# Optimization experiments

Hardware: AMD Instinct MI355X
Metric: run time of the kernel (lower is better)

## Reference

```python
import jax, jax.numpy as jnp
import numpy as np
import math

B, CIN, COUT, K, R = 8, 128, 128, 7, 2
GC = 16                     # group_channels (init arg `groups`)
G = COUT // GC              # number of dynamic-weight groups = 8
H = W = 32
EPS = 1e-5


def c4_lift(w):
    # w: [o, i, 4] -> dense 1x1 weight [o*4, i*4] via cyclic C4 shifts
    # torch: weight[:, r] = w[..., roll-by-r]  (e.g. r=1 -> [3,0,1,2])
    Wr = jnp.stack([jnp.roll(w, r, axis=-1) for r in range(4)], axis=1)  # [o,4,i,4]
    o, _, i, _ = Wr.shape
    return Wr.reshape(o * 4, i * 4)


def setup_inputs() -> dict:
    key = jax.random.key(0)
    ks = jax.random.split(key, 4)
    sc = 1.0 / math.sqrt(4 * CIN / 2)
    x = jax.random.normal(ks[0], (B, CIN * 4, H, W), dtype=jnp.float32)
    v_w = jax.random.normal(ks[1], (COUT, CIN, 4), dtype=jnp.float32) * sc
    c1_w = jax.random.normal(ks[2], (CIN // R, CIN, 4), dtype=jnp.float32) * sc
    gn_g = jnp.ones((CIN // R * 4,), jnp.float32)
    gn_b = jnp.zeros((CIN // R * 4,), jnp.float32)
    c2_w = jax.random.normal(ks[3], (K * K * G, CIN // R), dtype=jnp.float32) * (1.0 / math.sqrt(CIN // R))
    c2_b = jnp.zeros((K * K * G,), jnp.float32)
    return {"x": x, "v_w": v_w, "c1_w": c1_w, "gn_g": gn_g, "gn_b": gn_b, "c2_w": c2_w, "c2_b": c2_b}


def _forward(x, v_w, c1_w, gn_g, gn_b, c2_w, c2_b):
    b, _, h, w = x.shape
    # conv1: C4-equivariant 1x1
    t = jnp.einsum('oc,bchw->bohw', c4_lift(c1_w), x)        # [b, (CIN//R)*4, h, w]
    # GroupNorm(num_groups=CIN//R) -> normalize each group of 4 channels over (4,h,w)
    tr = t.reshape(b, CIN // R, 4, h, w)
    mu = tr.mean(axis=(2, 3, 4), keepdims=True)
    var = tr.var(axis=(2, 3, 4), keepdims=True)
    t = ((tr - mu) * jax.lax.rsqrt(var + EPS)).reshape(b, CIN // R * 4, h, w)
    t = jax.nn.relu(t * gn_g[None, :, None, None] + gn_b[None, :, None, None])
    # conv2: Conv3d 1x1 over the (c, 4) view
    tv = t.reshape(b, CIN // R, 4, h, w)
    wmap = jnp.einsum('oc,bcrhw->borhw', c2_w, tv) + c2_b[None, :, None, None, None]
    wmap = wmap.reshape(b, G, K, K, 4, h, w)
    # rotate the KxK kernel by r*90deg for C4 element r (r=0 identity)
    wmap = jnp.stack([jnp.rot90(wmap[:, :, :, :, r], k=r, axes=(2, 3)) for r in range(4)], axis=4)
    wmap = wmap.reshape(b, G, K * K, 4, h, w)                 # [b, g, p, r, h, w]
    # v branch (C4 1x1) + unfold (im2col, pad (K-1)//2, stride 1)
    v = jnp.einsum('oc,bchw->bohw', c4_lift(v_w), x)          # [b, COUT*4, h, w]
    p = (K - 1) // 2
    vp = jnp.pad(v, ((0, 0), (0, 0), (p, p), (p, p)))
    patches = jnp.stack([vp[:, :, i:i + h, j:j + w] for i in range(K) for j in range(K)], axis=2)
    patches = patches.reshape(b, G, GC, 4, K * K, h, w)       # [b, g, c, r, p, h, w]
    out = jnp.einsum('bgprhw,bgcrphw->bgcrhw', wmap, patches)
    return out.reshape(b, COUT * 4, h, w)


def reference(x, v_w, c1_w, gn_g, gn_b, c2_w, c2_b):
    return _forward(x, v_w, c1_w, gn_g, gn_b, c2_w, c2_b)
```

## Files before the change

### kernel.cpp

```cpp
#include <hip/hip_runtime.h>

#define BB   8
#define CIN  128
#define COUT 128
#define KS   7
#define HH   32
#define WWID 32
#define HW   1024
#define NG   8
#define GC   16
#define MROWS 768
#define TROWS 256
#define VROWS 512
#define KDIM 512
#define WMAP_O 392
#define WMAP_OP 448
#define C2K  64

#define AS1 __attribute__((address_space(1)))
#define AS3 __attribute__((address_space(3)))

typedef __attribute__((ext_vector_type(8))) short bf16x8;
typedef __attribute__((ext_vector_type(4))) float f32x4;

__device__ __forceinline__ short f2bf(float f) {
    unsigned u = __builtin_bit_cast(unsigned, f);
    u += 0x7fff + ((u >> 16) & 1);
    return (short)(u >> 16);
}
__device__ __forceinline__ float bf2f(unsigned short u) {
    unsigned v = (unsigned)u << 16;
    return __builtin_bit_cast(float, v);
}

__global__ __launch_bounds__(256) void prep_kernel(
    const float* __restrict__ x, const float* __restrict__ v_w,
    const float* __restrict__ c1_w, const float* __restrict__ c2_w,
    const float* __restrict__ c2_b,
    short* __restrict__ XT, short* __restrict__ Wb,
    short* __restrict__ c2wb, float* __restrict__ c2bp,
    float* __restrict__ gnstat)
{
    __shared__ short t[64][66];
    int bx = blockIdx.x, tid = threadIdx.x;
    if (bx < 1024) {
        int b = bx >> 7, c0 = ((bx >> 4) & 7) * 64, n0 = (bx & 15) * 64;
        const float* xb = x + ((size_t)b * KDIM + c0) * HW + n0;
        #pragma unroll
        for (int l = 0; l < 16; ++l) {
            int flat = l * 256 + tid;
            int row = flat >> 6, col = flat & 63;
            t[col][row] = f2bf(xb[(size_t)row * HW + col]);
        }
        __syncthreads();
        short* xt = XT + ((size_t)b * HW + n0) * KDIM + c0;
        #pragma unroll
        for (int l = 0; l < 8; ++l) {
            int u = l * 256 + tid;
            int nrow = u >> 5, cp = (u & 31) * 2;
            short2 v = make_short2(t[nrow][cp], t[nrow][cp + 1]);
            *(short2*)(xt + (size_t)nrow * KDIM + cp) = v;
        }
    } else if (bx < 2560) {
        int idx = (bx - 1024) * 256 + tid;
        int row = idx >> 9, col = idx & 511;
        int i = col >> 2, s = col & 3;
        float val;
        if (row < 256) {
            int o = row >> 2, r = row & 3;
            val = c1_w[(o * CIN + i) * 4 + ((s - r) & 3)];
        } else {
            int ro = row - 256;
            int o = ro >> 2, r = ro & 3;
            val = v_w[(o * CIN + i) * 4 + ((s - r) & 3)];
        }
        Wb[idx] = f2bf(val);
    } else if (bx < 2672) {
        int idx = (bx - 2560) * 256 + tid;
        int o = idx >> 6, k = idx & 63;
        c2wb[idx] = f2bf(o < WMAP_O ? c2_w[o * C2K + k] : 0.f);
        if (idx < WMAP_OP)
            c2bp[idx] = idx < WMAP_O ? c2_b[idx] : 0.f;
    } else {
        *(float4*)(gnstat + tid * 4) = make_float4(0.f, 0.f, 0.f, 0.f);
    }
}

#define GBM 64
#define GBN 128
#define GBK 64
__global__ __launch_bounds__(256) void gemm_mfma_kernel(
    const short* __restrict__ Wb, const short* __restrict__ XT,
    short* __restrict__ tvb, float* __restrict__ gnstat)
{
    __shared__ short As[2][GBM * GBK];
    __shared__ short Bs[2][GBN * GBK];
    int b  = blockIdx.z;
    int m0 = blockIdx.y * GBM;
    int n0 = blockIdx.x * GBN;
    int tid = threadIdx.x;
    int lane = tid & 63, wv = tid >> 6;
    int wm = wv & 1, wn = wv >> 1;
    int rl = lane & 15, kg = lane >> 4;
    const short* Ab = Wb + (size_t)m0 * KDIM;
    const short* Bb = XT + ((size_t)b * HW + n0) * KDIM;
    f32x4 acc[2][4] = {};

#define GEMM_STAGE(buf, k0)                                                              \
    do {                                                                                 \
        _Pragma("unroll")                                                                \
        for (int l = 0; l < 2; ++l) {                                                    \
            int c = l * 256 + tid;                                                       \
            int row = c >> 3, kc = c & 7;                                                \
            int kcs = kc ^ (row & 7);                                                    \
            __builtin_amdgcn_global_load_lds(                                            \
                (const AS1 void*)(Ab + (size_t)row * KDIM + (k0) + kcs * 8),             \
                (AS3 void*)(As[buf] + (l * 256 + wv * 64) * 8), 16, 0, 0);               \
        }                                                                                \
        _Pragma("unroll")                                                                \
        for (int l = 0; l < 4; ++l) {                                                    \
            int c = l * 256 + tid;                                                       \
            int row = c >> 3, kc = c & 7;                                                \
            int kcs = kc ^ (row & 7);                                                    \
            __builtin_amdgcn_global_load_lds(                                            \
                (const AS1 void*)(Bb + (size_t)row * KDIM + (k0) + kcs * 8),             \
                (AS3 void*)(Bs[buf] + (l * 256 + wv * 64) * 8), 16, 0, 0);               \
        }                                                                                \
    } while (0)

    GEMM_STAGE(0, 0);
    __syncthreads();
    for (int t = 0; t < KDIM / GBK; ++t) {
        int cur = t & 1;
        if (t < KDIM / GBK - 1) GEMM_STAGE(cur ^ 1, (t + 1) * GBK);
        #pragma unroll
        for (int ks = 0; ks < 2; ++ks) {
            bf16x8 af[2], bfr[4];
            #pragma unroll
            for (int mf = 0; mf < 2; ++mf) {
                int row = wm * 32 + mf * 16 + rl;
                af[mf] = *(const bf16x8*)(As[cur] + row * GBK + ((ks * 4 + kg) ^ (row & 7)) * 8);
            }
            #pragma unroll
            for (int nf = 0; nf < 4; ++nf) {
                int row = wn * 64 + nf * 16 + rl;
                bfr[nf] = *(const bf16x8*)(Bs[cur] + row * GBK + ((ks * 4 + kg) ^ (row & 7)) * 8);
            }
            #pragma unroll
            for (int mf = 0; mf < 2; ++mf)
                #pragma unroll
                for (int nf = 0; nf < 4; ++nf)
                    acc[mf][nf] = __builtin_amdgcn_mfma_f32_16x16x32_bf16(af[mf], bfr[nf], acc[mf][nf], 0, 0, 0);
        }
        __syncthreads();
    }
#undef GEMM_STAGE

    short* Cb = tvb + (size_t)b * MROWS * HW;
    #pragma unroll
    for (int mf = 0; mf < 2; ++mf) {
        int rowb = m0 + wm * 32 + mf * 16 + kg * 4;
        #pragma unroll
        for (int nf = 0; nf < 4; ++nf) {
            int col = n0 + wn * 64 + nf * 16 + rl;
            #pragma unroll
            for (int i = 0; i < 4; ++i)
                Cb[(size_t)(rowb + i) * HW + col] = f2bf(acc[mf][nf][i]);
        }
    }

    if (m0 < TROWS) {
        #pragma unroll
        for (int mf = 0; mf < 2; ++mf) {
            float s = 0.f, sq = 0.f;
            #pragma unroll
            for (int nf = 0; nf < 4; ++nf)
                #pragma unroll
                for (int i = 0; i < 4; ++i) {
                    float v = acc[mf][nf][i];
                    s += v; sq += v * v;
                }
            #pragma unroll
            for (int m = 1; m <= 8; m <<= 1) {
                s  += __shfl_xor(s, m);
                sq += __shfl_xor(sq, m);
            }
            if (rl == 0) {
                int grp = (m0 + wm * 32 + mf * 16 + kg * 4) >> 2;
                atomicAdd(&gnstat[(b * 64 + grp) * 2],     s);
                atomicAdd(&gnstat[(b * 64 + grp) * 2 + 1], sq);
            }
        }
    }
}

__global__ __launch_bounds__(256) void tkn2_kernel(
    const short* __restrict__ tvb, const float* __restrict__ gnstat,
    const float* __restrict__ gn_g, const float* __restrict__ gn_b,
    short* __restrict__ tn)
{
    __shared__ short ts[64][72];
    __shared__ float sc[64], sh[64];
    int b4r = blockIdx.x;
    int b = b4r >> 2, r = b4r & 3;
    int hw0 = blockIdx.y * 64;
    int tid = threadIdx.x;
    if (tid < 64) {
        float s   = gnstat[(b * 64 + tid) * 2];
        float sq  = gnstat[(b * 64 + tid) * 2 + 1];
        float mu  = s * (1.f / 4096.f);
        float var = sq * (1.f / 4096.f) - mu * mu;
        float inv = rsqrtf(var + 1e-5f);
        int ch = tid * 4 + r;
        float g = gn_g[ch], bb = gn_b[ch];
        sc[tid] = inv * g;
        sh[tid] = bb - mu * inv * g;
    }
    #pragma unroll
    for (int l = 0; l < 16; ++l) {
        int flat = l * 256 + tid;
        int c = flat >> 6, hw = flat & 63;
        ts[c][hw] = tvb[((size_t)b * MROWS + c * 4 + r) * HW + hw0 + hw];
    }
    __syncthreads();
    #pragma unroll
    for (int l = 0; l < 2; ++l) {
        int u = l * 256 + tid;
        int hw = u >> 3, c0 = (u & 7) * 8;
        bf16x8 v;
        #pragma unroll
        for (int j = 0; j < 8; ++j) {
            float f = bf2f((unsigned short)ts[c0 + j][hw]);
            f = fmaxf(f * sc[c0 + j] + sh[c0 + j], 0.f);
            v[j] = f2bf(f);
        }
        *(bf16x8*)(tn + ((size_t)b4r * HW + hw0 + hw) * C2K + c0) = v;
    }
}

__global__ __launch_bounds__(256) void wmap3_kernel(
    const short* __restrict__ c2wb, const short* __restrict__ tn,
    const float* __restrict__ c2bp, short* __restrict__ wmapB)
{
    __shared__ short As[64 * 64];
    __shared__ short Bs[128 * 64];
    int n0  = blockIdx.x * 128;
    int m0  = blockIdx.y * 64;
    int b4r = blockIdx.z;
    int tid = threadIdx.x;
    int lane = tid & 63, wv = tid >> 6;
    int wm = wv & 1, wn = wv >> 1;
    int rl = lane & 15, kg = lane >> 4;
    const short* Bb = tn + ((size_t)b4r * HW + n0) * C2K;

    #pragma unroll
    for (int l = 0; l < 2; ++l) {
        int c = l * 256 + tid;
        int row = c >> 3, kc = c & 7;
        int kcs = kc ^ (row & 7);
        __builtin_amdgcn_global_load_lds(
            (const AS1 void*)(c2wb + (size_t)(m0 + row) * C2K + kcs * 8),
            (AS3 void*)(As + (l * 256 + wv * 64) * 8), 16, 0, 0);
    }
    #pragma unroll
    for (int l = 0; l < 4; ++l) {
        int c = l * 256 + tid;
        int row = c >> 3, kc = c & 7;
        int kcs = kc ^ (row & 7);
        __builtin_amdgcn_global_load_lds(
            (const AS1 void*)(Bb + (size_t)row * C2K + kcs * 8),
            (AS3 void*)(Bs + (l * 256 + wv * 64) * 8), 16, 0, 0);
    }
    __syncthreads();

    f32x4 acc[2][4] = {};
    #pragma unroll
    for (int ks = 0; ks < 2; ++ks) {
        bf16x8 af[2], bfr[4];
        #pragma unroll
        for (int mf = 0; mf < 2; ++mf) {
            int row = wm * 32 + mf * 16 + rl;
            af[mf] = *(const bf16x8*)(As + row * 64 + ((ks * 4 + kg) ^ (row & 7)) * 8);
        }
        #pragma unroll
        for (int nf = 0; nf < 4; ++nf) {
            int row = wn * 64 + nf * 16 + rl;
            bfr[nf] = *(const bf16x8*)(Bs + row * 64 + ((ks * 4 + kg) ^ (row & 7)) * 8);
        }
        #pragma unroll
        for (int mf = 0; mf < 2; ++mf)
            #pragma unroll
            for (int nf = 0; nf < 4; ++nf)
                acc[mf][nf] = __builtin_amdgcn_mfma_f32_16x16x32_bf16(af[mf], bfr[nf], acc[mf][nf], 0, 0, 0);
    }

    short* wb = wmapB + (size_t)b4r * WMAP_OP * HW;
    #pragma unroll
    for (int mf = 0; mf < 2; ++mf) {
        int rowb = m0 + wm * 32 + mf * 16 + kg * 4;
        float bi[4];
        #pragma unroll
        for (int i = 0; i < 4; ++i) bi[i] = c2bp[rowb + i];
        #pragma unroll
        for (int nf = 0; nf < 4; ++nf) {
            int col = n0 + wn * 64 + nf * 16 + rl;
            #pragma unroll
            for (int i = 0; i < 4; ++i)
                wb[(size_t)(rowb + i) * HW + col] = f2bf(acc[mf][nf][i] + bi[i]);
        }
    }
}

__global__ __launch_bounds__(256, 3) void agg5_kernel(
    const short* __restrict__ tvb, const short* __restrict__ wmapB,
    float* __restrict__ out)
{
    __shared__ float vt[16][15][44];
    int bx = blockIdx.x;
    int b = bx >> 5;
    int g = (bx >> 2) & 7;
    int r = bx & 3;
    int h0  = blockIdx.y * 8;
    int tid = threadIdx.x;
    int w0q = tid & 7, hb = (tid >> 3) & 1, cc4 = (tid >> 4) & 3, cq = tid >> 6;
    int hl = cq * 2 + hb;
    int h = h0 + hl, w0 = w0q * 4;

    int A, Bc, Cc;
    if      (r == 0) { A = 0;  Bc = 7;  Cc = 1;  }
    else if (r == 1) { A = 6;  Bc = -1; Cc = 7;  }
    else if (r == 2) { A = 48; Bc = -7; Cc = -1; }
    else             { A = 42; Bc = 1;  Cc = -7; }

    const short* vpb = tvb + ((size_t)b * MROWS + TROWS) * HW;
    for (int e = tid; e < 16 * 15 * 3; e += 256) {
        int cc  = e / 45;
        int rem = e - cc * 45;
        int row = rem / 3, q = rem - row * 3;
        int col = (q == 0) ? 0 : (36 + (q - 1) * 4);
        *(float4*)(&vt[cc][row][col]) = make_float4(0.f, 0.f, 0.f, 0.f);
    }
    for (int f = tid; f < 16 * 15 * 8; f += 256) {
        int cc  = f / 120;
        int rem = f - cc * 120;
        int row = rem >> 3, q = rem & 7;
        int gh = h0 - 3 + row;
        float4 v4 = make_float4(0.f, 0.f, 0.f, 0.f);
        if (gh >= 0 && gh < HH) {
            int ch = (g * GC + cc) * 4 + r;
            ushort4 u = *(const ushort4*)(vpb + (size_t)ch * HW + gh * WWID + q * 4);
            v4 = make_float4(bf2f(u.x), bf2f(u.y), bf2f(u.z), bf2f(u.w));
        }
        *(float4*)(&vt[cc][row][4 + q * 4]) = v4;
    }
    __syncthreads();

    const short* wmb = wmapB + ((size_t)(b * 4 + r) * WMAP_OP + g * 49) * HW + h * WWID + w0;
    float acc[4][4] = {};
    #pragma unroll
    for (int di = 0; di < 7; ++di) {
        float wrf[7][4];
        #pragma unroll
        for (int dj = 0; dj < 7; ++dj) {
            int porig = A + Bc * di + Cc * dj;
            ushort4 wv = *(const ushort4*)(wmb + (size_t)porig * HW);
            wrf[dj][0] = bf2f(wv.x); wrf[dj][1] = bf2f(wv.y);
            wrf[dj][2] = bf2f(wv.z); wrf[dj][3] = bf2f(wv.w);
        }
        #pragma unroll
        for (int c2 = 0; c2 < 4; ++c2) {
            int hc = cc4 * 4 + c2;
            const float* rp = &vt[hc][hl + di][w0];
            float4 q0 = *(const float4*)(rp);
            float4 q1 = *(const float4*)(rp + 4);
            float4 q2 = *(const float4*)(rp + 8);
            float win[12] = {q0.x, q0.y, q0.z, q0.w,
                             q1.x, q1.y, q1.z, q1.w,
                             q2.x, q2.y, q2.z, q2.w};
            #pragma unroll
            for (int dj = 0; dj < 7; ++dj)
                #pragma unroll
                for (int px = 0; px < 4; ++px)
                    acc[c2][px] += wrf[dj][px] * win[px + dj + 1];
        }
    }
    #pragma unroll
    for (int c2 = 0; c2 < 4; ++c2) {
        int ch = (g * GC + cc4 * 4 + c2) * 4 + r;
        float4 o4 = make_float4(acc[c2][0], acc[c2][1], acc[c2][2], acc[c2][3]);
        *(float4*)(out + ((size_t)b * 512 + ch) * HW + h * WWID + w0) = o4;
    }
}

extern "C" void kernel_launch(void* const* d_in, const int* in_sizes, int n_in,
                              void* d_out, int out_size, void* d_ws, size_t ws_size,
                              hipStream_t stream)
{
    const float* x    = (const float*)d_in[0];
    const float* v_w  = (const float*)d_in[1];
    const float* c1_w = (const float*)d_in[2];
    const float* gn_g = (const float*)d_in[3];
    const float* gn_b = (const float*)d_in[4];
    const float* c2_w = (const float*)d_in[5];
    const float* c2_b = (const float*)d_in[6];
    float* out = (float*)d_out;

    char* p = (char*)d_ws;
    short* Wb     = (short*)p;           p += (size_t)MROWS * KDIM * 2;
    short* tvb    = (short*)p;           p += (size_t)BB * MROWS * HW * 2;
    short* wmapB  = (short*)p;           p += (size_t)32 * WMAP_OP * HW * 2;
    short* XT     = (short*)wmapB;
    short* tn     = (short*)p;           p += (size_t)32 * HW * C2K * 2;
    short* c2wb   = (short*)p;           p += (size_t)WMAP_OP * C2K * 2;
    float* c2bp   = (float*)p;           p += (size_t)WMAP_OP * 4;
    float* gnstat = (float*)p;           p += (size_t)512 * 2 * 4;

    prep_kernel     <<<2673, 256, 0, stream>>>(x, v_w, c1_w, c2_w, c2_b, XT, Wb, c2wb, c2bp, gnstat);
    gemm_mfma_kernel<<<dim3(HW / GBN, MROWS / GBM, BB), 256, 0, stream>>>(Wb, XT, tvb, gnstat);
    tkn2_kernel     <<<dim3(32, 16), 256, 0, stream>>>(tvb, gnstat, gn_g, gn_b, tn);
    wmap3_kernel    <<<dim3(HW / 128, WMAP_OP / 64, 32), 256, 0, stream>>>(c2wb, tn, c2bp, wmapB);
    agg5_kernel     <<<dim3(BB * NG * 4, 4), 256, 0, stream>>>(tvb, wmapB, out);
}
```

Baseline: 64.33 us.

## Stage wmap GEMM output through LDS for coalesced stores; split aggregation channels

The wmap GEMM epilogue now writes the bf16 results into shared memory and then stores them to global memory as contiguous 16-byte rows. It also skips the padded rows past 392. Previously each lane wrote scattered 2-byte elements. The aggregation kernel is split over a new grid z dimension, so each block handles 8 of the 16 channels, with a smaller LDS tile and a higher occupancy hint. The split doubles the block count and raises parallelism, but each wmap weight row is now loaded twice, once per half.

```diff
diff --git a/kernel.cpp b/kernel.cpp
--- a/kernel.cpp
+++ b/kernel.cpp
@@ -242,8 +242,10 @@
     const short* __restrict__ c2wb, const short* __restrict__ tn,
     const float* __restrict__ c2bp, short* __restrict__ wmapB)
 {
-    __shared__ short As[64 * 64];
-    __shared__ short Bs[128 * 64];
+    __shared__ short smem[64 * 64 + 128 * 64];
+    short* As = smem;
+    short* Bs = smem + 64 * 64;
+    short* Ps = smem;
     int n0  = blockIdx.x * 128;
     int m0  = blockIdx.y * 64;
     int b4r = blockIdx.z;
@@ -293,35 +295,47 @@
             for (int nf = 0; nf < 4; ++nf)
                 acc[mf][nf] = __builtin_amdgcn_mfma_f32_16x16x32_bf16(af[mf], bfr[nf], acc[mf][nf], 0, 0, 0);
     }
-
-    short* wb = wmapB + (size_t)b4r * WMAP_OP * HW;
+    __syncthreads();
+
     #pragma unroll
     for (int mf = 0; mf < 2; ++mf) {
-        int rowb = m0 + wm * 32 + mf * 16 + kg * 4;
+        int rowl = wm * 32 + mf * 16 + kg * 4;
         float bi[4];
         #pragma unroll
-        for (int i = 0; i < 4; ++i) bi[i] = c2bp[rowb + i];
+        for (int i = 0; i < 4; ++i) bi[i] = c2bp[m0 + rowl + i];
         #pragma unroll
         for (int nf = 0; nf < 4; ++nf) {
-            int col = n0 + wn * 64 + nf * 16 + rl;
+            int col = wn * 64 + nf * 16 + rl;
             #pragma unroll
             for (int i = 0; i < 4; ++i)
-                wb[(size_t)(rowb + i) * HW + col] = f2bf(acc[mf][nf][i] + bi[i]);
-        }
-    }
-}
-
-__global__ __launch_bounds__(256, 3) void agg5_kernel(
+                Ps[(rowl + i) * 136 + col] = f2bf(acc[mf][nf][i] + bi[i]);
+        }
+    }
+    __syncthreads();
+
+    int row = tid >> 2, segl = tid & 3;
+    if (m0 + row < WMAP_O) {
+        short* dst = wmapB + (size_t)b4r * WMAP_OP * HW + (size_t)(m0 + row) * HW + n0;
+        #pragma unroll
+        for (int s2 = 0; s2 < 4; ++s2) {
+            int col = segl * 8 + s2 * 32;
+            *(bf16x8*)(dst + col) = *(const bf16x8*)(Ps + row * 136 + col);
+        }
+    }
+}
+
+__global__ __launch_bounds__(256, 5) void agg6_kernel(
     const short* __restrict__ tvb, const short* __restrict__ wmapB,
     float* __restrict__ out)
 {
-    __shared__ float vt[16][15][44];
+    __shared__ float vt[8][15][44];
     int bx = blockIdx.x;
     int b = bx >> 5;
     int g = (bx >> 2) & 7;
     int r = bx & 3;
-    int h0  = blockIdx.y * 8;
-    int tid = threadIdx.x;
+    int h0   = blockIdx.y * 8;
+    int half = blockIdx.z;
+    int tid  = threadIdx.x;
     int w0q = tid & 7, hb = (tid >> 3) & 1, cc4 = (tid >> 4) & 3, cq = tid >> 6;
     int hl = cq * 2 + hb;
     int h = h0 + hl, w0 = w0q * 4;
@@ -333,21 +347,21 @@
     else             { A = 42; Bc = 1;  Cc = -7; }
 
     const short* vpb = tvb + ((size_t)b * MROWS + TROWS) * HW;
-    for (int e = tid; e < 16 * 15 * 3; e += 256) {
+    for (int e = tid; e < 8 * 15 * 3; e += 256) {
         int cc  = e / 45;
         int rem = e - cc * 45;
         int row = rem / 3, q = rem - row * 3;
         int col = (q == 0) ? 0 : (36 + (q - 1) * 4);
         *(float4*)(&vt[cc][row][col]) = make_float4(0.f, 0.f, 0.f, 0.f);
     }
-    for (int f = tid; f < 16 * 15 * 8; f += 256) {
+    for (int f = tid; f < 8 * 15 * 8; f += 256) {
         int cc  = f / 120;
         int rem = f - cc * 120;
         int row = rem >> 3, q = rem & 7;
         int gh = h0 - 3 + row;
         float4 v4 = make_float4(0.f, 0.f, 0.f, 0.f);
         if (gh >= 0 && gh < HH) {
-            int ch = (g * GC + cc) * 4 + r;
+            int ch = (g * GC + half * 8 + cc) * 4 + r;
             ushort4 u = *(const ushort4*)(vpb + (size_t)ch * HW + gh * WWID + q * 4);
             v4 = make_float4(bf2f(u.x), bf2f(u.y), bf2f(u.z), bf2f(u.w));
         }
@@ -356,7 +370,7 @@
     __syncthreads();
 
     const short* wmb = wmapB + ((size_t)(b * 4 + r) * WMAP_OP + g * 49) * HW + h * WWID + w0;
-    float acc[4][4] = {};
+    float acc[2][4] = {};
     #pragma unroll
     for (int di = 0; di < 7; ++di) {
         float wrf[7][4];
@@ -368,8 +382,8 @@
             wrf[dj][2] = bf2f(wv.z); wrf[dj][3] = bf2f(wv.w);
         }
         #pragma unroll
-        for (int c2 = 0; c2 < 4; ++c2) {
-            int hc = cc4 * 4 + c2;
+        for (int c2 = 0; c2 < 2; ++c2) {
+            int hc = cc4 * 2 + c2;
             const float* rp = &vt[hc][hl + di][w0];
             float4 q0 = *(const float4*)(rp);
             float4 q1 = *(const float4*)(rp + 4);
@@ -385,8 +399,8 @@
         }
     }
     #pragma unroll
-    for (int c2 = 0; c2 < 4; ++c2) {
-        int ch = (g * GC + cc4 * 4 + c2) * 4 + r;
+    for (int c2 = 0; c2 < 2; ++c2) {
+        int ch = (g * GC + half * 8 + cc4 * 2 + c2) * 4 + r;
         float4 o4 = make_float4(acc[c2][0], acc[c2][1], acc[c2][2], acc[c2][3]);
         *(float4*)(out + ((size_t)b * 512 + ch) * HW + h * WWID + w0) = o4;
     }
@@ -419,5 +433,5 @@
     gemm_mfma_kernel<<<dim3(HW / GBN, MROWS / GBM, BB), 256, 0, stream>>>(Wb, XT, tvb, gnstat);
     tkn2_kernel     <<<dim3(32, 16), 256, 0, stream>>>(tvb, gnstat, gn_g, gn_b, tn);
     wmap3_kernel    <<<dim3(HW / 128, WMAP_OP / 64, 32), 256, 0, stream>>>(c2wb, tn, c2bp, wmapB);
-    agg5_kernel     <<<dim3(BB * NG * 4, 4), 256, 0, stream>>>(tvb, wmapB, out);
-}
+    agg6_kernel     <<<dim3(BB * NG * 4, 4, 2), 256, 0, stream>>>(tvb, wmapB, out);
+}
```

Result: faster. 61.36 us, median of 2 (-4.6%).
